# Performance work log

Measured on AMD Instinct MI355X. Metric: run time of the kernel, lower is better.

The kernel has to match this reference:

```python
import jax, jax.numpy as jnp
import numpy as np

B = 16384       # batch size
NT = 26         # number of embedding tables
NROWS = 100000  # rows per table
M = 128         # embedding dim == bottom MLP output dim
BOT = [13, 512, 256, 128]
TOP = [479, 1024, 1024, 512, 256, 1]


def _linear_params(k, n, m):
    kw, kb = jax.random.split(k)
    W = jax.random.normal(kw, (m, n), jnp.float32) * np.sqrt(2.0 / (m + n))
    b = jax.random.normal(kb, (m,), jnp.float32) * np.sqrt(1.0 / m)
    return W, b


def setup_inputs() -> dict:
    key = jax.random.key(0)
    ks = jax.random.split(key, 16)
    dense_x = jax.random.normal(ks[0], (B, 13), jnp.float32)
    lS_i = jax.random.randint(ks[1], (NT, B), 0, NROWS, dtype=jnp.int32)
    lS_o = jnp.tile(jnp.arange(B, dtype=jnp.int32), (NT, 1))  # 1 index per bag
    s = float(np.sqrt(1.0 / NROWS))
    emb = jax.random.uniform(ks[2], (NT, NROWS, M), jnp.float32, -s, s)
    d = {"dense_x": dense_x, "lS_o": lS_o, "lS_i": lS_i, "emb": emb}
    for i in range(3):
        W, b = _linear_params(ks[3 + i], BOT[i], BOT[i + 1])
        d[f"bw{i}"] = W; d[f"bb{i}"] = b
    for i in range(5):
        W, b = _linear_params(ks[6 + i], TOP[i], TOP[i + 1])
        d[f"tw{i}"] = W; d[f"tb{i}"] = b
    return d


def _emb_bag_sum(table, idx, off):
    # nn.EmbeddingBag(mode='sum'): bag k sums rows idx[off[k]:off[k+1]]
    L = idx.shape[0]
    bag = jnp.searchsorted(off, jnp.arange(L, dtype=off.dtype), side='right') - 1
    return jax.ops.segment_sum(table[idx], bag, num_segments=B)  # [B, M]


def _forward(dense_x, emb, bws, bbs, tws, tbs, lS_o, lS_i):
    # bottom MLP (all ReLU, sigmoid_bot=-1)
    x = dense_x
    for W, b in zip(bws, bbs):
        x = jax.nn.relu(x @ W.T + b)
    # multi-table embedding-bag sum pooling
    ly = jax.vmap(_emb_bag_sum)(emb, lS_i, lS_o)          # [NT, B, M]
    # dot interaction
    T = jnp.concatenate([x[None], ly], axis=0).transpose(1, 0, 2)  # [B, NT+1, M]
    Z = jnp.einsum('bim,bjm->bij', T, T)                  # [B, 27, 27]
    li, lj = jnp.tril_indices(NT + 1, k=-1)               # pairs i>j, torch order
    Zflat = Z[:, li, lj]                                  # [B, 351]
    z = jnp.concatenate([x, Zflat], axis=1)               # [B, 479]
    # top MLP: ReLU except Sigmoid at layer index 4 (sigmoid_top=4)
    for i, (W, b) in enumerate(zip(tws, tbs)):
        z = z @ W.T + b
        z = jax.nn.sigmoid(z) if i == 4 else jax.nn.relu(z)
    return z


def reference(dense_x, lS_o, lS_i, emb,
              bw0, bb0, bw1, bb1, bw2, bb2,
              tw0, tb0, tw1, tb1, tw2, tb2, tw3, tb3, tw4, tb4):
    return _forward(dense_x, emb,
                    [bw0, bw1, bw2], [bb0, bb1, bb2],
                    [tw0, tw1, tw2, tw3, tw4], [tb0, tb1, tb2, tb3, tb4],
                    lS_o, lS_i)
```

## Files before the change

### kernel.cpp

```cpp
#include <hip/hip_runtime.h>
#include <cstdint>
#include <cstddef>

typedef _Float16 h16;
typedef __attribute__((ext_vector_type(8))) _Float16 half8;
typedef __attribute__((ext_vector_type(4))) _Float16 half4;
typedef __attribute__((ext_vector_type(2))) _Float16 half2v;
typedef __attribute__((ext_vector_type(4))) float f32x4;
typedef __attribute__((ext_vector_type(2))) float f32x2;

#define NB 16384
#define NTAB 26
#define NR 100000

__device__ __forceinline__ void gload16(const void* g, void* l) {
  __builtin_amdgcn_global_load_lds(
      (const __attribute__((address_space(1))) unsigned int*)g,
      (__attribute__((address_space(3))) unsigned int*)l, 16, 0, 0);
}

__global__ __launch_bounds__(256) void cvt_bot0_k(
    const float* __restrict__ s0, const float* __restrict__ s1,
    const float* __restrict__ s2, const float* __restrict__ s3,
    const float* __restrict__ s4, const float* __restrict__ s5,
    h16* __restrict__ dst, const float* __restrict__ x,
    const float* __restrict__ W0, const float* __restrict__ b0,
    h16* __restrict__ Y) {
  __shared__ float xs[32][14];
  int b = blockIdx.x;
  if (b >= 9344) {
    const int bb = b - 9344;
    const int row0 = bb * 32;
    const int tid = threadIdx.x;
    for (int i = tid; i < 32 * 13; i += 256) {
      int r = i / 13, k = i - r * 13;
      xs[r][k] = x[(size_t)(row0 + r) * 13 + k];
    }
    float w0[13], w1[13];
#pragma unroll
    for (int k = 0; k < 13; ++k) {
      w0[k] = W0[tid * 13 + k];
      w1[k] = W0[(tid + 256) * 13 + k];
    }
    const float bz0 = b0[tid], bz1 = b0[tid + 256];
    __syncthreads();
    for (int r = 0; r < 32; ++r) {
      float a0 = bz0, a1 = bz1;
#pragma unroll
      for (int k = 0; k < 13; ++k) {
        const float xv = xs[r][k];
        a0 += xv * w0[k];
        a1 += xv * w1[k];
      }
      Y[(size_t)(row0 + r) * 512 + tid] = (h16)fmaxf(a0, 0.f);
      Y[(size_t)(row0 + r) * 512 + tid + 256] = (h16)fmaxf(a1, 0.f);
    }
    return;
  }
  const float* src; int K, kl, i0; size_t doff;
  if (b < 512)       { src=s0; K=512;  kl=9;  i0=(b-0)*256;    doff=0; }
  else if (b < 640)  { src=s1; K=256;  kl=8;  i0=(b-512)*256;  doff=131072; }
  else if (b < 2688) { src=s2; K=479;  kl=9;  i0=(b-640)*256;  doff=163840; }
  else if (b < 6784) { src=s3; K=1024; kl=10; i0=(b-2688)*256; doff=688128; }
  else if (b < 8832) { src=s4; K=1024; kl=10; i0=(b-6784)*256; doff=1736704; }
  else               { src=s5; K=512;  kl=9;  i0=(b-8832)*256; doff=2260992; }
  int i = i0 + threadIdx.x;
  int n = i >> kl, k = i & ((1 << kl) - 1);
  dst[doff + i] = (k < K) ? (h16)src[(size_t)n * K + k] : (h16)0.f;
}

__global__ __launch_bounds__(256, 2) void mid_k(
    const h16* __restrict__ Y0, const h16* __restrict__ W1,
    const float* __restrict__ b1, const h16* __restrict__ W2,
    const float* __restrict__ b2, h16* __restrict__ Xc) {
  __shared__ __align__(16) h16 Sa[32 * 64];
  __shared__ __align__(16) h16 Sb[256 * 64];
  __shared__ __align__(16) h16 Y1[32 * 264];
  const int tid = threadIdx.x;
  const int lane = tid & 63;
  const int w = tid >> 6;
  const int l15 = lane & 15;
  const int kq = lane >> 4;
  const int l7 = lane & 7;
  const size_t row0 = (size_t)blockIdx.x * 32;

  const int srow = tid >> 3;
  const int sch = (tid & 7) ^ (srow & 7);
  const h16* gA = Y0 + (row0 + srow) * 512 + sch * 8;
  const h16* gB = W1 + (size_t)srow * 512 + sch * 8;

  f32x4 acc[2][4] = {};
  for (int t = 0; t < 8; ++t) {
    const int k0 = t * 64;
    gload16(gA + k0, Sa + tid * 8);
#pragma unroll
    for (int i = 0; i < 8; ++i)
      gload16(gB + (size_t)(i * 32) * 512 + k0, Sb + i * 2048 + tid * 8);
    __syncthreads();
#pragma unroll
    for (int kk = 0; kk < 2; ++kk) {
      const int kb = kk * 4 + kq;
      const int sl = (kb ^ l7) << 3;
      half8 a[2], bfr[4];
#pragma unroll
      for (int mi = 0; mi < 2; ++mi)
        a[mi] = *(const half8*)&Sa[(mi * 16 + l15) * 64 + sl];
#pragma unroll
      for (int ni = 0; ni < 4; ++ni)
        bfr[ni] = *(const half8*)&Sb[(w * 64 + ni * 16 + l15) * 64 + sl];
#pragma unroll
      for (int mi = 0; mi < 2; ++mi)
#pragma unroll
        for (int ni = 0; ni < 4; ++ni)
          acc[mi][ni] = __builtin_amdgcn_mfma_f32_16x16x32_f16(bfr[ni], a[mi], acc[mi][ni], 0, 0, 0);
    }
    __syncthreads();
  }

#pragma unroll
  for (int mi = 0; mi < 2; ++mi) {
    const int row = mi * 16 + l15;
#pragma unroll
    for (int ni = 0; ni < 4; ++ni) {
      const int col = w * 64 + ni * 16 + kq * 4;
      const f32x4 bv = *(const f32x4*)&b1[col];
      half4 h;
#pragma unroll
      for (int ri = 0; ri < 4; ++ri)
        h[ri] = (h16)fmaxf(acc[mi][ni][ri] + bv[ri], 0.f);
      *(half4*)&Y1[row * 264 + col] = h;
    }
  }
  __syncthreads();

  f32x4 acc2[2][2] = {};
  for (int ks = 0; ks < 8; ++ks) {
    half8 av[2], bv[2];
#pragma unroll
    for (int mi = 0; mi < 2; ++mi)
      av[mi] = *(const half8*)&Y1[(mi * 16 + l15) * 264 + ks * 32 + kq * 8];
#pragma unroll
    for (int nf = 0; nf < 2; ++nf) {
      const int col = (w * 2 + nf) * 16 + l15;
      bv[nf] = *(const half8*)&W2[(size_t)col * 256 + ks * 32 + kq * 8];
    }
#pragma unroll
    for (int mi = 0; mi < 2; ++mi)
#pragma unroll
      for (int nf = 0; nf < 2; ++nf)
        acc2[mi][nf] = __builtin_amdgcn_mfma_f32_16x16x32_f16(bv[nf], av[mi], acc2[mi][nf], 0, 0, 0);
  }
#pragma unroll
  for (int mi = 0; mi < 2; ++mi) {
    const size_t row = row0 + mi * 16 + l15;
#pragma unroll
    for (int nf = 0; nf < 2; ++nf) {
      const int col = (w * 2 + nf) * 16 + kq * 4;
      const f32x4 bv = *(const f32x4*)&b2[col];
      half4 h;
#pragma unroll
      for (int ri = 0; ri < 4; ++ri)
        h[ri] = (h16)fmaxf(acc2[mi][nf][ri] + bv[ri], 0.f);
      *(half4*)&Xc[row * 128 + col] = h;
    }
  }
}

template <int GYL>
__global__ __launch_bounds__(256, 4) void gemm_sb(
    const h16* __restrict__ A, const h16* __restrict__ W,
    const float* __restrict__ bias, h16* __restrict__ C, int N, int K) {
  __shared__ __align__(16) h16 As[128 * 64];
  __shared__ __align__(16) h16 Bs[128 * 64];
  const int b = blockIdx.x;
  const int c8 = b & 7;
  const int q = b >> 3;
  const int jcol = q & ((1 << GYL) - 1);
  const int krow = ((q >> GYL) << 3) | c8;
  const int tid = threadIdx.x;
  const int lane = tid & 63;
  const int wave = tid >> 6;
  const int wm = wave >> 1, wn = wave & 1;
  const size_t row0 = (size_t)krow * 128;
  const size_t col0 = (size_t)jcol * 128;
  const int lr = lane >> 3;
  const int swzc = (((lane & 7) ^ lr) << 3);
  const int l15 = lane & 15;
  const int kq = lane >> 4;
  const int l7 = lane & 7;
  const int nt = K >> 6;

  const h16* ga = A + (row0 + wave * 32 + lr) * (size_t)K + swzc;
  const h16* gb = W + (col0 + wave * 32 + lr) * (size_t)K + swzc;

  f32x4 acc[4][4] = {};

  for (int t = 0; t < nt; ++t) {
    const int k0 = t << 6;
    h16* la = As + wave * 2048;
    h16* lb = Bs + wave * 2048;
#pragma unroll
    for (int i = 0; i < 4; ++i) {
      gload16(ga + (size_t)i * 8 * K + k0, la + i * 512);
      gload16(gb + (size_t)i * 8 * K + k0, lb + i * 512);
    }
    __syncthreads();
#pragma unroll
    for (int kk = 0; kk < 2; ++kk) {
      half8 a[4], bfr[4];
      const int kb = kk * 4 + kq;
#pragma unroll
      for (int mi = 0; mi < 4; ++mi)
        a[mi] = *(const half8*)&As[(wm * 64 + mi * 16 + l15) * 64 + ((kb ^ l7) << 3)];
#pragma unroll
      for (int ni = 0; ni < 4; ++ni)
        bfr[ni] = *(const half8*)&Bs[(wn * 64 + ni * 16 + l15) * 64 + ((kb ^ l7) << 3)];
#pragma unroll
      for (int mi = 0; mi < 4; ++mi)
#pragma unroll
        for (int ni = 0; ni < 4; ++ni)
          acc[mi][ni] = __builtin_amdgcn_mfma_f32_16x16x32_f16(a[mi], bfr[ni], acc[mi][ni], 0, 0, 0);
    }
    __syncthreads();
  }

#pragma unroll
  for (int mi = 0; mi < 4; ++mi)
#pragma unroll
    for (int ni = 0; ni < 4; ++ni) {
      const size_t col = col0 + wn * 64 + ni * 16 + l15;
      const float bv = bias[col];
#pragma unroll
      for (int ri = 0; ri < 4; ++ri) {
        const size_t row = row0 + wm * 64 + mi * 16 + kq * 4 + ri;
        float v = acc[mi][ni][ri] + bv;
        C[row * N + col] = (h16)fmaxf(v, 0.f);
      }
    }
}

template <int GYL>
__global__ __launch_bounds__(256, 4) void gemm_sb64(
    const h16* __restrict__ A, const h16* __restrict__ W,
    const float* __restrict__ bias, h16* __restrict__ C, int N, int K) {
  __shared__ __align__(16) h16 As[64 * 64];
  __shared__ __align__(16) h16 Bs[128 * 64];
  const int b = blockIdx.x;
  const int c8 = b & 7;
  const int q = b >> 3;
  const int jcol = q & ((1 << GYL) - 1);
  const int krow = ((q >> GYL) << 3) | c8;
  const int tid = threadIdx.x;
  const int lane = tid & 63;
  const int wave = tid >> 6;
  const int wm = wave >> 1, wn = wave & 1;
  const size_t row0 = (size_t)krow * 64;
  const size_t col0 = (size_t)jcol * 128;
  const int l15 = lane & 15;
  const int kq = lane >> 4;
  const int l7 = lane & 7;
  const int nt = K >> 6;

  const int srow = tid >> 3;
  const int sch = (tid & 7) ^ (srow & 7);
  const h16* ga = A + (row0 + srow) * (size_t)K + sch * 8;
  const h16* gb = W + (col0 + srow) * (size_t)K + sch * 8;

  f32x4 acc[2][4] = {};

  for (int t = 0; t < nt; ++t) {
    const int k0 = t << 6;
#pragma unroll
    for (int i = 0; i < 2; ++i)
      gload16(ga + (size_t)(i * 32) * K + k0, As + i * 2048 + tid * 8);
#pragma unroll
    for (int i = 0; i < 4; ++i)
      gload16(gb + (size_t)(i * 32) * K + k0, Bs + i * 2048 + tid * 8);
    __syncthreads();
#pragma unroll
    for (int kk = 0; kk < 2; ++kk) {
      const int kb = kk * 4 + kq;
      const int sl = (kb ^ l7) << 3;
      half8 a[2], bfr[4];
#pragma unroll
      for (int mi = 0; mi < 2; ++mi)
        a[mi] = *(const half8*)&As[(wm * 32 + mi * 16 + l15) * 64 + sl];
#pragma unroll
      for (int ni = 0; ni < 4; ++ni)
        bfr[ni] = *(const half8*)&Bs[(wn * 64 + ni * 16 + l15) * 64 + sl];
#pragma unroll
      for (int mi = 0; mi < 2; ++mi)
#pragma unroll
        for (int ni = 0; ni < 4; ++ni)
          acc[mi][ni] = __builtin_amdgcn_mfma_f32_16x16x32_f16(a[mi], bfr[ni], acc[mi][ni], 0, 0, 0);
    }
    __syncthreads();
  }

#pragma unroll
  for (int mi = 0; mi < 2; ++mi)
#pragma unroll
    for (int ni = 0; ni < 4; ++ni) {
      const size_t col = col0 + wn * 64 + ni * 16 + l15;
      const float bv = bias[col];
#pragma unroll
      for (int ri = 0; ri < 4; ++ri) {
        const size_t row = row0 + wm * 32 + mi * 16 + kq * 4 + ri;
        float v = acc[mi][ni][ri] + bv;
        C[row * N + col] = (h16)fmaxf(v, 0.f);
      }
    }
}

__global__ __launch_bounds__(256, 4) void gemm_t3s(
    const h16* __restrict__ A, const h16* __restrict__ W,
    const float* __restrict__ bias, const float* __restrict__ w4,
    const float* __restrict__ b4, float* __restrict__ out) {
  const int K = 512;
  __shared__ __align__(16) h16 As[32 * 64];
  __shared__ __align__(16) h16 Bs[256 * 64];
  __shared__ float red[4][32];
  const int tid = threadIdx.x;
  const int lane = tid & 63;
  const int w = tid >> 6;
  const int l15 = lane & 15;
  const int kq = lane >> 4;
  const int l7 = lane & 7;
  const size_t row0 = (size_t)blockIdx.x * 32;

  const int srow = tid >> 3;
  const int sch = (tid & 7) ^ (srow & 7);
  const h16* gA = A + (row0 + srow) * (size_t)K + sch * 8;
  const h16* gB = W + (size_t)srow * K + sch * 8;

  f32x4 acc[2][4] = {};
  for (int t = 0; t < 8; ++t) {
    const int k0 = t * 64;
    gload16(gA + k0, As + tid * 8);
#pragma unroll
    for (int i = 0; i < 8; ++i)
      gload16(gB + (size_t)(i * 32) * K + k0, Bs + i * 2048 + tid * 8);
    __syncthreads();
#pragma unroll
    for (int kk = 0; kk < 2; ++kk) {
      const int kb = kk * 4 + kq;
      const int sl = (kb ^ l7) << 3;
      half8 a[2], bfr[4];
#pragma unroll
      for (int mi = 0; mi < 2; ++mi)
        a[mi] = *(const half8*)&As[(mi * 16 + l15) * 64 + sl];
#pragma unroll
      for (int ni = 0; ni < 4; ++ni)
        bfr[ni] = *(const half8*)&Bs[(w * 64 + ni * 16 + l15) * 64 + sl];
#pragma unroll
      for (int mi = 0; mi < 2; ++mi)
#pragma unroll
        for (int ni = 0; ni < 4; ++ni)
          acc[mi][ni] = __builtin_amdgcn_mfma_f32_16x16x32_f16(a[mi], bfr[ni], acc[mi][ni], 0, 0, 0);
    }
    __syncthreads();
  }

#pragma unroll
  for (int mi = 0; mi < 2; ++mi) {
    float s[4] = {0.f, 0.f, 0.f, 0.f};
#pragma unroll
    for (int ni = 0; ni < 4; ++ni) {
      const int col = w * 64 + ni * 16 + l15;
      const float bv = bias[col];
      const float wv = w4[col];
#pragma unroll
      for (int ri = 0; ri < 4; ++ri)
        s[ri] += fmaxf(acc[mi][ni][ri] + bv, 0.f) * wv;
    }
#pragma unroll
    for (int ri = 0; ri < 4; ++ri) {
      float v = s[ri];
      v += __shfl_xor(v, 1);
      v += __shfl_xor(v, 2);
      v += __shfl_xor(v, 4);
      v += __shfl_xor(v, 8);
      if (l15 == 0) red[w][mi * 16 + kq * 4 + ri] = v;
    }
  }
  __syncthreads();
  if (tid < 32) {
    float v = red[0][tid] + red[1][tid] + red[2][tid] + red[3][tid] + b4[0];
    out[row0 + tid] = 1.f / (1.f + expf(-v));
  }
}

__global__ __launch_bounds__(256) void interact_k(
    const h16* __restrict__ X, const float* __restrict__ emb,
    const int* __restrict__ lSi, h16* __restrict__ z) {
  __shared__ __align__(16) h16 T[4][32][136];
  const int lane = threadIdx.x & 63;
  const int wv = threadIdx.x >> 6;
  const size_t b = (size_t)blockIdx.x * 4 + wv;

  int idxs[NTAB];
#pragma unroll
  for (int t = 0; t < NTAB; ++t) idxs[t] = lSi[t * NB + (int)b];

  for (int i = lane; i < 5 * 128; i += 64)
    T[wv][27 + (i >> 7)][i & 127] = (h16)0.f;

  {
    half2v v = *(const half2v*)(X + b * 128 + lane * 2);
    *(half2v*)&T[wv][0][lane * 2] = v;
    *(half2v*)(z + b * 512 + lane * 2) = v;
  }
  const int thalf = lane >> 5;
  const int c4 = (lane & 31) * 4;
#pragma unroll
  for (int i = 0; i < NTAB / 2; ++i) {
    const int t = 2 * i + thalf;
    const f32x4 v = *(const f32x4*)(emb + ((size_t)t * NR + idxs[t]) * 128 + c4);
    half4 h;
#pragma unroll
    for (int j = 0; j < 4; ++j) h[j] = (h16)v[j];
    *(half4*)&T[wv][1 + t][c4] = h;
  }

  __syncthreads();

  f32x4 acc00 = {}, acc10 = {}, acc11 = {};
  const int l15 = lane & 15;
  const int kq = lane >> 4;
#pragma unroll
  for (int kk = 0; kk < 4; ++kk) {
    const int ko = kk * 32 + kq * 8;
    half8 a0 = *(const half8*)&T[wv][l15][ko];
    half8 a1 = *(const half8*)&T[wv][16 + l15][ko];
    acc00 = __builtin_amdgcn_mfma_f32_16x16x32_f16(a0, a0, acc00, 0, 0, 0);
    acc10 = __builtin_amdgcn_mfma_f32_16x16x32_f16(a1, a0, acc10, 0, 0, 0);
    acc11 = __builtin_amdgcn_mfma_f32_16x16x32_f16(a1, a1, acc11, 0, 0, 0);
  }
  h16* zr = z + b * 512 + 128;
#pragma unroll
  for (int ri = 0; ri < 4; ++ri) {
    int i0 = kq * 4 + ri;
    int i1 = 16 + i0;
    if (l15 < i0) zr[i0 * (i0 - 1) / 2 + l15] = (h16)acc00[ri];
    if (i1 < 27) {
      zr[i1 * (i1 - 1) / 2 + l15] = (h16)acc10[ri];
      int j1 = 16 + l15;
      if (j1 < i1) zr[i1 * (i1 - 1) / 2 + j1] = (h16)acc11[ri];
    }
  }
}

extern "C" void kernel_launch(void* const* d_in, const int* in_sizes, int n_in,
                              void* d_out, int out_size, void* d_ws, size_t ws_size,
                              hipStream_t stream) {
  const float* dense_x = (const float*)d_in[0];
  const int* lSi = (const int*)d_in[2];
  const float* emb = (const float*)d_in[3];
  const float* bw0 = (const float*)d_in[4];
  const float* bb0 = (const float*)d_in[5];
  const float* bw1 = (const float*)d_in[6];
  const float* bb1 = (const float*)d_in[7];
  const float* bw2 = (const float*)d_in[8];
  const float* bb2 = (const float*)d_in[9];
  const float* tw0 = (const float*)d_in[10];
  const float* tb0 = (const float*)d_in[11];
  const float* tw1 = (const float*)d_in[12];
  const float* tb1 = (const float*)d_in[13];
  const float* tw2 = (const float*)d_in[14];
  const float* tb2 = (const float*)d_in[15];
  const float* tw3 = (const float*)d_in[16];
  const float* tb3 = (const float*)d_in[17];
  const float* tw4 = (const float*)d_in[18];
  const float* tb4 = (const float*)d_in[19];
  float* out = (float*)d_out;

  char* ws = (char*)d_ws;
  const size_t MB = (size_t)1 << 20;
  h16* Y0 = (h16*)(ws + 0 * MB);
  h16* Xc = (h16*)(ws + 24 * MB);
  h16* Zz = (h16*)(ws + 32 * MB);
  h16* U0 = (h16*)(ws + 48 * MB);
  h16* U1 = (h16*)(ws + 0 * MB);
  h16* U2 = (h16*)(ws + 32 * MB);
  h16* w1p = (h16*)(ws + 80 * MB);
  h16* w2p = w1p + 256 * 512;
  h16* t0p = w2p + 128 * 256;
  h16* t1p = t0p + 1024 * 512;
  h16* t2p = t1p + 1024 * 1024;
  h16* t3p = t2p + 512 * 1024;
  (void)in_sizes; (void)n_in; (void)out_size; (void)ws_size;

  cvt_bot0_k<<<9344 + 512, 256, 0, stream>>>(bw1, bw2, tw0, tw1, tw2, tw3,
                                             w1p, dense_x, bw0, bb0, Y0);
  mid_k<<<512, 256, 0, stream>>>(Y0, w1p, bb1, w2p, bb2, Xc);
  interact_k<<<NB / 4, 256, 0, stream>>>(Xc, emb, lSi, Zz);
  gemm_sb<3><<<128 * 8, 256, 0, stream>>>(Zz, t0p, tb0, U0, 1024, 512);
  gemm_sb<3><<<128 * 8, 256, 0, stream>>>(U0, t1p, tb1, U1, 1024, 1024);
  gemm_sb64<2><<<256 * 4, 256, 0, stream>>>(U1, t2p, tb2, U2, 512, 1024);
  gemm_t3s<<<512, 256, 0, stream>>>(U2, t3p, tb3, tw4, tb4, out);
}
```

Measured before the change: 177.4 us.

## Fuse bottom MLP layer 0 into mid kernel, keeping activations in LDS

The first bottom-MLP layer (13->512) moves out of the conversion kernel and into mid_k. Each block now computes its 32 rows of Y0 directly into shared memory and feeds them to the layer-1 MFMA loop. This removes the 16 MB fp16 Y0 round trip through global memory and the per-tile A loads. In exchange, mid_k uses more LDS (Y1 aliases the Y0 buffer) and loses the XOR swizzle on its A-operand reads, which may cause LDS bank conflicts. Occupancy may also drop.

Result: faster. 169.4 us (-4.6%).

```diff
diff --git a/kernel.cpp b/kernel.cpp
--- a/kernel.cpp
+++ b/kernel.cpp
@@ -19,44 +19,12 @@
       (__attribute__((address_space(3))) unsigned int*)l, 16, 0, 0);
 }
 
-__global__ __launch_bounds__(256) void cvt_bot0_k(
+__global__ __launch_bounds__(256) void cvt_all_k(
     const float* __restrict__ s0, const float* __restrict__ s1,
     const float* __restrict__ s2, const float* __restrict__ s3,
     const float* __restrict__ s4, const float* __restrict__ s5,
-    h16* __restrict__ dst, const float* __restrict__ x,
-    const float* __restrict__ W0, const float* __restrict__ b0,
-    h16* __restrict__ Y) {
-  __shared__ float xs[32][14];
+    h16* __restrict__ dst) {
   int b = blockIdx.x;
-  if (b >= 9344) {
-    const int bb = b - 9344;
-    const int row0 = bb * 32;
-    const int tid = threadIdx.x;
-    for (int i = tid; i < 32 * 13; i += 256) {
-      int r = i / 13, k = i - r * 13;
-      xs[r][k] = x[(size_t)(row0 + r) * 13 + k];
-    }
-    float w0[13], w1[13];
-#pragma unroll
-    for (int k = 0; k < 13; ++k) {
-      w0[k] = W0[tid * 13 + k];
-      w1[k] = W0[(tid + 256) * 13 + k];
-    }
-    const float bz0 = b0[tid], bz1 = b0[tid + 256];
-    __syncthreads();
-    for (int r = 0; r < 32; ++r) {
-      float a0 = bz0, a1 = bz1;
-#pragma unroll
-      for (int k = 0; k < 13; ++k) {
-        const float xv = xs[r][k];
-        a0 += xv * w0[k];
-        a1 += xv * w1[k];
-      }
-      Y[(size_t)(row0 + r) * 512 + tid] = (h16)fmaxf(a0, 0.f);
-      Y[(size_t)(row0 + r) * 512 + tid + 256] = (h16)fmaxf(a1, 0.f);
-    }
-    return;
-  }
   const float* src; int K, kl, i0; size_t doff;
   if (b < 512)       { src=s0; K=512;  kl=9;  i0=(b-0)*256;    doff=0; }
   else if (b < 640)  { src=s1; K=256;  kl=8;  i0=(b-512)*256;  doff=131072; }
@@ -70,12 +38,14 @@
 }
 
 __global__ __launch_bounds__(256, 2) void mid_k(
-    const h16* __restrict__ Y0, const h16* __restrict__ W1,
+    const float* __restrict__ x, const float* __restrict__ W0,
+    const float* __restrict__ b0, const h16* __restrict__ W1,
     const float* __restrict__ b1, const h16* __restrict__ W2,
     const float* __restrict__ b2, h16* __restrict__ Xc) {
-  __shared__ __align__(16) h16 Sa[32 * 64];
+  __shared__ __align__(16) h16 Y0s[32 * 520];
   __shared__ __align__(16) h16 Sb[256 * 64];
-  __shared__ __align__(16) h16 Y1[32 * 264];
+  __shared__ float xs[32][14];
+  h16* Y1 = Y0s;
   const int tid = threadIdx.x;
   const int lane = tid & 63;
   const int w = tid >> 6;
@@ -84,15 +54,38 @@
   const int l7 = lane & 7;
   const size_t row0 = (size_t)blockIdx.x * 32;
 
+  for (int i = tid; i < 32 * 13; i += 256) {
+    int r = i / 13, k = i - r * 13;
+    xs[r][k] = x[(row0 + r) * 13 + k];
+  }
+  float w0[13], w1r[13];
+#pragma unroll
+  for (int k = 0; k < 13; ++k) {
+    w0[k] = W0[tid * 13 + k];
+    w1r[k] = W0[(tid + 256) * 13 + k];
+  }
+  const float bz0 = b0[tid], bz1 = b0[tid + 256];
+  __syncthreads();
+  for (int r = 0; r < 32; ++r) {
+    float a0 = bz0, a1 = bz1;
+#pragma unroll
+    for (int k = 0; k < 13; ++k) {
+      const float xv = xs[r][k];
+      a0 += xv * w0[k];
+      a1 += xv * w1r[k];
+    }
+    Y0s[r * 520 + tid] = (h16)fmaxf(a0, 0.f);
+    Y0s[r * 520 + tid + 256] = (h16)fmaxf(a1, 0.f);
+  }
+  __syncthreads();
+
   const int srow = tid >> 3;
   const int sch = (tid & 7) ^ (srow & 7);
-  const h16* gA = Y0 + (row0 + srow) * 512 + sch * 8;
   const h16* gB = W1 + (size_t)srow * 512 + sch * 8;
 
   f32x4 acc[2][4] = {};
   for (int t = 0; t < 8; ++t) {
     const int k0 = t * 64;
-    gload16(gA + k0, Sa + tid * 8);
 #pragma unroll
     for (int i = 0; i < 8; ++i)
       gload16(gB + (size_t)(i * 32) * 512 + k0, Sb + i * 2048 + tid * 8);
@@ -104,7 +97,7 @@
       half8 a[2], bfr[4];
 #pragma unroll
       for (int mi = 0; mi < 2; ++mi)
-        a[mi] = *(const half8*)&Sa[(mi * 16 + l15) * 64 + sl];
+        a[mi] = *(const half8*)&Y0s[(mi * 16 + l15) * 520 + k0 + kb * 8];
 #pragma unroll
       for (int ni = 0; ni < 4; ++ni)
         bfr[ni] = *(const half8*)&Sb[(w * 64 + ni * 16 + l15) * 64 + sl];
@@ -476,7 +469,6 @@
 
   char* ws = (char*)d_ws;
   const size_t MB = (size_t)1 << 20;
-  h16* Y0 = (h16*)(ws + 0 * MB);
   h16* Xc = (h16*)(ws + 24 * MB);
   h16* Zz = (h16*)(ws + 32 * MB);
   h16* U0 = (h16*)(ws + 48 * MB);
@@ -490,9 +482,8 @@
   h16* t3p = t2p + 512 * 1024;
   (void)in_sizes; (void)n_in; (void)out_size; (void)ws_size;
 
-  cvt_bot0_k<<<9344 + 512, 256, 0, stream>>>(bw1, bw2, tw0, tw1, tw2, tw3,
-                                             w1p, dense_x, bw0, bb0, Y0);
-  mid_k<<<512, 256, 0, stream>>>(Y0, w1p, bb1, w2p, bb2, Xc);
+  cvt_all_k<<<9344, 256, 0, stream>>>(bw1, bw2, tw0, tw1, tw2, tw3, w1p);
+  mid_k<<<512, 256, 0, stream>>>(dense_x, bw0, bb0, w1p, bb1, w2p, bb2, Xc);
   interact_k<<<NB / 4, 256, 0, stream>>>(Xc, emb, lSi, Zz);
   gemm_sb<3><<<128 * 8, 256, 0, stream>>>(Zz, t0p, tb0, U0, 1024, 512);
   gemm_sb<3><<<128 * 8, 256, 0, stream>>>(U0, t1p, tb1, U1, 1024, 1024);
```
